# Kernel tuning notes

Hardware: AMD Instinct MI355X
Metric: run time of the kernel (lower is better)

Reference implementation:

```python
import jax, jax.numpy as jnp
import numpy as np

H = 2048          # hidden_size
NH = 16           # num_attention_heads
D_NOPE = 64
D_ROPE = 64
D_V = 64
KV_RANK = 256
E = 8             # n_routed_experts
INTER = 1408      # moe_intermediate_size
EPS = 1e-6
THETA = 10000.0
B, S = 1, 2048
Q_HEAD = D_NOPE + D_ROPE


def rms_norm(x, w, eps=EPS):
    xf = x.astype(jnp.float32)
    var = jnp.mean(xf * xf, axis=-1, keepdims=True)
    return (w * (xf * jax.lax.rsqrt(var + eps))).astype(x.dtype)


def rotate_half(x):
    d = x.shape[-1] // 2
    return jnp.concatenate([-x[..., d:], x[..., :d]], axis=-1)


def rope_tables(seq_len, dim, theta=THETA):
    inv_freq = 1.0 / (theta ** (jnp.arange(0, dim, 2, dtype=jnp.float32) / dim))
    t = jnp.arange(seq_len, dtype=jnp.float32)
    freqs = jnp.outer(t, inv_freq)
    emb = jnp.concatenate([freqs, freqs], axis=-1)  # [S, dim]
    return jnp.cos(emb), jnp.sin(emb)


def setup_inputs() -> dict:
    key = jax.random.key(0)
    ks = jax.random.split(key, 10)
    sc = 0.02
    inp = {
        "positions": jnp.broadcast_to(jnp.arange(S, dtype=jnp.int32)[None, :], (B, S)),
        "hidden_states": jax.random.normal(ks[0], (B, S, H), dtype=jnp.float32),
        "input_ln_w": jnp.ones((H,), jnp.float32),
        "q_proj_w": jax.random.normal(ks[1], (NH * Q_HEAD, H), jnp.float32) * sc,
        "kv_a_w": jax.random.normal(ks[2], (KV_RANK + D_ROPE, H), jnp.float32) * sc,
        "kv_a_ln_w": jnp.ones((KV_RANK,), jnp.float32),
        "kv_b_w": jax.random.normal(ks[3], (NH * (D_NOPE + D_V), KV_RANK), jnp.float32) * sc,
        "o_proj_w": jax.random.normal(ks[4], (H, NH * D_V), jnp.float32) * sc,
        "post_ln_w": jnp.ones((H,), jnp.float32),
        "gate_w": jax.random.normal(ks[5], (E, H), jnp.float32) * sc,
        "fc1_w": jax.random.normal(ks[6], (E, INTER, H), jnp.float32) * sc,
        "fc2_w": jax.random.normal(ks[7], (E, H, INTER), jnp.float32) * sc,
    }
    return inp


def reference(positions, hidden_states, input_ln_w, q_proj_w, kv_a_w, kv_a_ln_w,
              kv_b_w, o_proj_w, post_ln_w, gate_w, fc1_w, fc2_w):
    x = hidden_states
    sa_in = rms_norm(x, input_ln_w)

    # Q projection -> [B, NH, S, D_NOPE + D_ROPE]
    q = (sa_in @ q_proj_w.T).reshape(B, S, NH, Q_HEAD).transpose(0, 2, 1, 3)
    q_nope, q_pe = q[..., :D_NOPE], q[..., D_NOPE:]

    # KV compression path
    ckv_pe = sa_in @ kv_a_w.T                       # [B, S, KV_RANK + D_ROPE]
    compressed_kv, k_pe = ckv_pe[..., :KV_RANK], ckv_pe[..., KV_RANK:]
    k_pe = k_pe.reshape(B, S, 1, D_ROPE).transpose(0, 2, 1, 3)  # [B,1,S,Dr]
    kv = (rms_norm(compressed_kv, kv_a_ln_w) @ kv_b_w.T)
    kv = kv.reshape(B, S, NH, D_NOPE + D_V).transpose(0, 2, 1, 3)
    k_nope, v = kv[..., :D_NOPE], kv[..., D_NOPE:]

    # RoPE on pe halves
    cos, sin = rope_tables(S, D_ROPE)
    cos_sel = cos[positions][:, None]               # [B,1,S,Dr]
    sin_sel = sin[positions][:, None]
    q_pe = q_pe * cos_sel + rotate_half(q_pe) * sin_sel
    k_pe = k_pe * cos_sel + rotate_half(k_pe) * sin_sel

    query = jnp.concatenate([q_nope, q_pe], axis=-1)                       # [B,NH,S,Dq]
    key = jnp.concatenate([k_nope, jnp.broadcast_to(k_pe, (B, NH, S, D_ROPE))], axis=-1)

    scale = Q_HEAD ** -0.5
    scores = jnp.einsum("bhqd,bhkd->bhqk", query, key) * scale
    causal = jnp.tril(jnp.ones((S, S), dtype=bool))
    scores = jnp.where(causal, scores, jnp.finfo(scores.dtype).min)
    attn = jax.nn.softmax(scores, axis=-1)
    ctx = jnp.einsum("bhqk,bhkd->bhqd", attn, v)                            # [B,NH,S,Dv]
    ctx = ctx.transpose(0, 2, 1, 3).reshape(B, S, NH * D_V)
    attn_out = ctx @ o_proj_w.T

    x = x + attn_out

    # dense all-expert MoE
    mlp_in = rms_norm(x, post_ln_w)
    probs = jax.nn.softmax(mlp_in @ gate_w.T, axis=-1)                      # [B,S,E]
    h = jax.nn.silu(jnp.einsum("bsd,eid->bsei", mlp_in, fc1_w))             # [B,S,E,INTER]
    moe_out = jnp.einsum("bse,bsei,ehi->bsh", probs, h, fc2_w)

    return x + moe_out
```

## Files before the change

kernel.cpp:

```cpp
#include <hip/hip_runtime.h>
#include <cstdint>
#include <cstddef>

typedef __bf16 bf16;
typedef __bf16 bf16x8 __attribute__((ext_vector_type(8)));
typedef float  f32x4  __attribute__((ext_vector_type(4)));

constexpr int S_      = 2048;
constexpr int H_      = 2048;
constexpr int NH_     = 16;
constexpr int KV_RANK_= 256;
constexpr int EXP_    = 8;
constexpr int INTER_  = 1408;
constexpr int QH_     = 128;
constexpr float EPS_  = 1e-6f;

__device__ inline void gload16(const void* g, void* l) {
  __builtin_amdgcn_global_load_lds(
      (const __attribute__((address_space(1))) void*)g,
      (__attribute__((address_space(3))) void*)l, 16, 0, 0);
}

enum { EPI_BF16 = 0, EPI_F32 = 1, EPI_ADD = 2, EPI_SILU = 3, EPI_ATOM = 4 };

template <int EPI, typename TB, int TILE>
__global__ void __launch_bounds__(256) gemm_bt(
    const bf16* __restrict__ A, const TB* __restrict__ B,
    void* __restrict__ Cv, const float* __restrict__ aux,
    int M, int N, int K, int lda, int ldb, int ldc, int flags,
    long zA, long zB, long zC, long auxZ, int auxRS,
    int kPerE, long bExpStride, int expBasePerZ)
{
  constexpr int FR = TILE / 32;
  if ((flags & 1) && blockIdx.x > blockIdx.y) return;
  const int tileN = blockIdx.x * TILE;
  const int tileM = blockIdx.y * TILE;
  const int z = blockIdx.z;
  A += (long)z * zA;

  __shared__ __align__(16) bf16 As[TILE * 64];
  __shared__ __align__(16) TB   Bs[TILE * 64];
  char* AsB = (char*)As;
  char* BsB = (char*)Bs;

  const int tid  = threadIdx.x;
  const int lane = tid & 63;
  const int wave = tid >> 6;
  const int wr = wave >> 1, wc = wave & 1;
  const int quad = lane >> 4, r16 = lane & 15;

  const int ldbe = (kPerE > 0) ? kPerE : ldb;
  const TB* BzBase = (kPerE > 0) ? (B + (long)z * expBasePerZ * bExpStride)
                                 : (B + (long)z * zB);

  constexpr int IA = TILE / 32;
  const bf16* aG[IA]; char* aL[IA];
#pragma unroll
  for (int i = 0; i < IA; i++) {
    int n = (wave * IA + i) * 64 + lane;
    int row = n >> 3, cp = n & 7;
    int cc = (cp ^ (row & 7)) << 3;
    int rowg = tileM + row; if (rowg > M - 1) rowg = M - 1;
    aG[i] = A + (long)rowg * lda + cc;
    aL[i] = AsB + (long)(wave * IA + i) * 1024;
  }
  constexpr int IB = (sizeof(TB) == 4) ? (TILE / 16) : (TILE / 32);
  const TB* bG[IB]; char* bL[IB];
#pragma unroll
  for (int i = 0; i < IB; i++) {
    int n = (wave * IB + i) * 64 + lane;
    int row, cc;
    if constexpr (sizeof(TB) == 4) { row = n >> 4; cc = ((n & 15) ^ (row & 15)) << 2; }
    else                           { row = n >> 3; cc = ((n & 7)  ^ (row & 7))  << 3; }
    int rowg = tileN + row; if (rowg > N - 1) rowg = N - 1;
    bG[i] = BzBase + (long)rowg * ldbe + cc;
    bL[i] = BsB + (long)(wave * IB + i) * 1024;
  }

  int aOff[FR], bOff[FR];
#pragma unroll
  for (int i = 0; i < FR; i++) {
    int row = wr * (TILE / 2) + i * 16 + r16;
    aOff[i] = row * 128 + ((quad ^ (row & 7)) << 4);
  }
#pragma unroll
  for (int j = 0; j < FR; j++) {
    int row = wc * (TILE / 2) + j * 16 + r16;
    if constexpr (sizeof(TB) == 4) bOff[j] = row * 256 + (((2 * quad) ^ (row & 15)) << 4);
    else                           bOff[j] = row * 128 + ((quad ^ (row & 7)) << 4);
  }

  f32x4 acc[FR][FR];
#pragma unroll
  for (int i = 0; i < FR; i++)
#pragma unroll
    for (int j = 0; j < FR; j++)
#pragma unroll
      for (int r = 0; r < 4; r++) acc[i][j][r] = 0.f;

  const int kEnd = (flags & 2) ? (tileM + TILE < K ? tileM + TILE : K) : K;
  int bk = 0; long eOff = 0;
  for (int k0 = 0; k0 < kEnd; k0 += 64) {
#pragma unroll
    for (int i = 0; i < IA; i++) gload16(aG[i] + k0, aL[i]);
#pragma unroll
    for (int i = 0; i < IB; i++) gload16(bG[i] + eOff + bk, bL[i]);
    __syncthreads();

#pragma unroll
    for (int s = 0; s < 2; s++) {
      bf16x8 af[FR], bfv[FR];
#pragma unroll
      for (int i = 0; i < FR; i++)
        af[i] = *(const bf16x8*)(AsB + (aOff[i] ^ (s << 6)));
#pragma unroll
      for (int j = 0; j < FR; j++) {
        if constexpr (sizeof(TB) == 2) {
          bfv[j] = *(const bf16x8*)(BsB + (bOff[j] ^ (s << 6)));
        } else {
          int a0 = bOff[j] ^ (s << 7);
          f32x4 lo = *(const f32x4*)(BsB + a0);
          f32x4 hi = *(const f32x4*)(BsB + (a0 ^ 16));
          bf16x8 v;
          v[0]=(bf16)lo[0]; v[1]=(bf16)lo[1]; v[2]=(bf16)lo[2]; v[3]=(bf16)lo[3];
          v[4]=(bf16)hi[0]; v[5]=(bf16)hi[1]; v[6]=(bf16)hi[2]; v[7]=(bf16)hi[3];
          bfv[j] = v;
        }
      }
#pragma unroll
      for (int i = 0; i < FR; i++)
#pragma unroll
        for (int j = 0; j < FR; j++)
          acc[i][j] = __builtin_amdgcn_mfma_f32_16x16x32_bf16(af[i], bfv[j], acc[i][j], 0, 0, 0);
    }
    __syncthreads();

    bk += 64;
    if (kPerE > 0 && bk >= kPerE) { bk = 0; eOff += bExpStride; }
  }

  bf16*  Cb = (bf16*)Cv + (long)z * zC;
  float* Cf = (float*)Cv + (long)z * zC;
  const float* auxp = aux + (long)z * auxZ;
  const int mB = tileM + wr * (TILE / 2) + quad * 4;
  const int nB = tileN + wc * (TILE / 2) + r16;
#pragma unroll
  for (int i = 0; i < FR; i++) {
#pragma unroll
    for (int r = 0; r < 4; r++) {
      int gm = mB + i * 16 + r;
      if (gm >= M) continue;
      float rowAux = 0.f;
      if constexpr (EPI == EPI_SILU) rowAux = auxp[(long)gm * auxRS];
#pragma unroll
      for (int j = 0; j < FR; j++) {
        int gn = nB + j * 16;
        if (gn >= N) continue;
        float v = acc[i][j][r];
        long off = (long)gm * ldc + gn;
        if constexpr (EPI == EPI_BF16)      Cb[off] = (bf16)v;
        else if constexpr (EPI == EPI_F32)  Cf[off] = v;
        else if constexpr (EPI == EPI_ADD)  Cf[off] = auxp[(long)gm * auxRS + gn] + v;
        else if constexpr (EPI == EPI_SILU) { float sv = v / (1.f + __expf(-v)); Cb[off] = (bf16)(sv * rowAux); }
        else                                atomicAdd(&Cf[off], v);
      }
    }
  }
}

template <int NIT>
__global__ void __launch_bounds__(256) rmsnorm_k(
    const float* __restrict__ x, const float* __restrict__ w,
    bf16* __restrict__ out, int inStride)
{
  const int row = blockIdx.x, tid = threadIdx.x;
  const float* xr = x + (long)row * inStride;
  float vals[NIT];
  float ss = 0.f;
#pragma unroll
  for (int i = 0; i < NIT; i++) { float v = xr[i * 256 + tid]; vals[i] = v; ss += v * v; }
#pragma unroll
  for (int o = 32; o; o >>= 1) ss += __shfl_xor(ss, o, 64);
  __shared__ float red[4];
  if ((tid & 63) == 0) red[tid >> 6] = ss;
  __syncthreads();
  ss = red[0] + red[1] + red[2] + red[3];
  const float rinv = rsqrtf(ss / (float)(NIT * 256) + EPS_);
  bf16* orow = out + (long)row * (NIT * 256);
#pragma unroll
  for (int i = 0; i < NIT; i++) { int c = i * 256 + tid; orow[c] = (bf16)(w[c] * vals[i] * rinv); }
}

__global__ void prep_qkv_k(const bf16* __restrict__ q, const bf16* __restrict__ kv,
                           const float* __restrict__ ckv, const int* __restrict__ pos,
                           bf16* __restrict__ query, bf16* __restrict__ key,
                           bf16* __restrict__ vvT)
{
  const int s = blockIdx.x, h = blockIdx.y, d = threadIdx.x;
  const long qkOff = ((long)h * S_ + s) * QH_ + d;
  if (d < 64) {
    query[qkOff] = q[(long)s * H_ + h * QH_ + d];
    key[qkOff]   = kv[(long)s * H_ + h * QH_ + d];
    vvT[((long)h * 64 + d) * S_ + s] = kv[(long)s * H_ + h * QH_ + 64 + d];
  } else {
    const int i = d - 64;
    const float p = (float)pos[s];
    const float invf = powf(10000.f, -(float)(2 * (i & 31)) / 64.f);
    const float ang = p * invf;
    const float cc = cosf(ang), sn = sinf(ang);
    const float xq  = (float)q[(long)s * H_ + h * QH_ + 64 + i];
    const float xqr = (i < 32) ? -(float)q[(long)s * H_ + h * QH_ + 64 + i + 32]
                               :  (float)q[(long)s * H_ + h * QH_ + 64 + i - 32];
    query[qkOff] = (bf16)(xq * cc + xqr * sn);
    const float xk  = ckv[(long)s * 320 + 256 + i];
    const float xkr = (i < 32) ? -ckv[(long)s * 320 + 256 + i + 32]
                               :  ckv[(long)s * 320 + 256 + i - 32];
    key[qkOff] = (bf16)(xk * cc + xkr * sn);
  }
}

__global__ void __launch_bounds__(256) softmax_causal_k(bf16* __restrict__ sc, long zStride, float scale)
{
  const int row = blockIdx.x, tid = threadIdx.x;
  bf16* p = sc + (long)blockIdx.y * zStride + (long)row * S_;
  float vals[8];
  float mx = -1e30f;
#pragma unroll
  for (int i = 0; i < 8; i++) {
    int c = i * 256 + tid;
    float v = (c <= row) ? (float)p[c] * scale : -1e30f;
    vals[i] = v; mx = fmaxf(mx, v);
  }
#pragma unroll
  for (int o = 32; o; o >>= 1) mx = fmaxf(mx, __shfl_xor(mx, o, 64));
  __shared__ float redA[4], redB[4];
  if ((tid & 63) == 0) redA[tid >> 6] = mx;
  __syncthreads();
  mx = fmaxf(fmaxf(redA[0], redA[1]), fmaxf(redA[2], redA[3]));
  float sum = 0.f;
#pragma unroll
  for (int i = 0; i < 8; i++) { float e = __expf(vals[i] - mx); vals[i] = e; sum += e; }
#pragma unroll
  for (int o = 32; o; o >>= 1) sum += __shfl_xor(sum, o, 64);
  if ((tid & 63) == 0) redB[tid >> 6] = sum;
  __syncthreads();
  sum = redB[0] + redB[1] + redB[2] + redB[3];
  const float rinv = 1.f / sum;
  const int lim = ((row >> 6) + 1) << 6;
#pragma unroll
  for (int i = 0; i < 8; i++) {
    int c = i * 256 + tid;
    if (c < lim) p[c] = (bf16)((c <= row) ? vals[i] * rinv : 0.f);
  }
}

__global__ void __launch_bounds__(256) gate_k(const bf16* __restrict__ mlp,
                                              const float* __restrict__ gw,
                                              float* __restrict__ probs)
{
  const int s = blockIdx.x, tid = threadIdx.x;
  float acc[8];
#pragma unroll
  for (int e = 0; e < 8; e++) acc[e] = 0.f;
  for (int c = tid; c < H_; c += 256) {
    float x = (float)mlp[(long)s * H_ + c];
#pragma unroll
    for (int e = 0; e < 8; e++) acc[e] += x * gw[e * H_ + c];
  }
  __shared__ float red[4][8];
#pragma unroll
  for (int e = 0; e < 8; e++) {
    float v = acc[e];
#pragma unroll
    for (int o = 32; o; o >>= 1) v += __shfl_xor(v, o, 64);
    if ((tid & 63) == 0) red[tid >> 6][e] = v;
  }
  __syncthreads();
  if (tid == 0) {
    float l[8]; float mx = -1e30f;
#pragma unroll
    for (int e = 0; e < 8; e++) { l[e] = red[0][e] + red[1][e] + red[2][e] + red[3][e]; mx = fmaxf(mx, l[e]); }
    float sum = 0.f;
#pragma unroll
    for (int e = 0; e < 8; e++) { l[e] = __expf(l[e] - mx); sum += l[e]; }
    float r = 1.f / sum;
#pragma unroll
    for (int e = 0; e < 8; e++) probs[(long)s * 8 + e] = l[e] * r;
  }
}

__global__ void __launch_bounds__(256) wconv_k(const float* __restrict__ in,
                                               bf16* __restrict__ out, int n8)
{
  int i = blockIdx.x * 256 + threadIdx.x;
  if (i < n8) {
    f32x4 a = ((const f32x4*)in)[2 * i];
    f32x4 b = ((const f32x4*)in)[2 * i + 1];
    bf16x8 v;
    v[0] = (bf16)a[0]; v[1] = (bf16)a[1]; v[2] = (bf16)a[2]; v[3] = (bf16)a[3];
    v[4] = (bf16)b[0]; v[5] = (bf16)b[1]; v[6] = (bf16)b[2]; v[7] = (bf16)b[3];
    ((bf16x8*)out)[i] = v;
  }
}

extern "C" void kernel_launch(void* const* d_in, const int* in_sizes, int n_in,
                              void* d_out, int out_size, void* d_ws, size_t ws_size,
                              hipStream_t stream)
{
  const int*   positions = (const int*)  d_in[0];
  const float* hidden    = (const float*)d_in[1];
  const float* ln1       = (const float*)d_in[2];
  const float* wq        = (const float*)d_in[3];
  const float* wkva      = (const float*)d_in[4];
  const float* lnkv      = (const float*)d_in[5];
  const float* wkvb      = (const float*)d_in[6];
  const float* wo        = (const float*)d_in[7];
  const float* ln2       = (const float*)d_in[8];
  const float* wg        = (const float*)d_in[9];
  const float* wfc1      = (const float*)d_in[10];
  const float* wfc2      = (const float*)d_in[11];
  float* out = (float*)d_out;

  char* wsb = (char*)d_ws;
  size_t off = 0;
  auto alloc = [&](size_t bytes) -> void* {
    void* p = wsb + off;
    off += (bytes + 255) & ~(size_t)255;
    return p;
  };
  bf16*  sa_in = (bf16*) alloc((size_t)S_ * H_ * 2);
  bf16*  qb    = (bf16*) alloc((size_t)S_ * H_ * 2);
  float* ckv   = (float*)alloc((size_t)S_ * 320 * 4);
  bf16*  ckvn  = (bf16*) alloc((size_t)S_ * KV_RANK_ * 2);
  bf16*  kvb   = (bf16*) alloc((size_t)S_ * H_ * 2);
  bf16*  query = (bf16*) alloc((size_t)NH_ * S_ * QH_ * 2);
  bf16*  key   = (bf16*) alloc((size_t)NH_ * S_ * QH_ * 2);
  bf16*  vvT   = (bf16*) alloc((size_t)NH_ * 64 * S_ * 2);
  bf16*  ctx   = (bf16*) alloc((size_t)S_ * NH_ * 64 * 2);
  bf16*  mlp   = (bf16*) alloc((size_t)S_ * H_ * 2);
  float* probs = (float*)alloc((size_t)S_ * 8 * 4);
  bf16*  hbuf  = (bf16*) alloc((size_t)S_ * EXP_ * INTER_ * 2);

  const size_t MBy = (size_t)1 << 20;
  const size_t rem = (ws_size > off) ? ws_size - off : 0;
  const size_t szSS   = (size_t)S_ * S_ * 2;
  const size_t szMoeW = (size_t)EXP_ * INTER_ * H_ * 2;

  int tier;
  if      (rem >= 136 * MBy) tier = 1;
  else if (rem >=  94 * MBy) tier = 2;
  else                       tier = 3;
  const bool cw = (tier <= 2);
  const int nz = (tier == 1) ? 16 : (tier == 2 ? 4 : 1);

  char* R = (char*)alloc(tier == 1 ? 16 * szSS : (tier == 2 ? 2 * szMoeW : szSS));
  bf16* scores = (bf16*)R;
  bf16* fc1b   = (bf16*)R;
  bf16* fc2b   = (bf16*)(R + szMoeW);
  bf16* wqb   = (bf16*)hbuf;
  bf16* wkvab = wqb   + (size_t)H_ * H_;
  bf16* wkvbb = wkvab + (size_t)320 * H_;
  bf16* wob   = wkvbb + (size_t)H_ * KV_RANK_;

  const float scale = 0.08838834764831845f;
  const long zQ = (long)S_ * QH_, zS = (long)S_ * S_, zV = (long)64 * S_;

  rmsnorm_k<8><<<S_, 256, 0, stream>>>(hidden, ln1, sa_in, H_);

  if (cw) {
    wconv_k<<<(H_*H_/8 + 255)/256, 256, 0, stream>>>(wq, wqb, H_*H_/8);
    wconv_k<<<(320*H_/8 + 255)/256, 256, 0, stream>>>(wkva, wkvab, 320*H_/8);
    wconv_k<<<(H_*KV_RANK_/8 + 255)/256, 256, 0, stream>>>(wkvb, wkvbb, H_*KV_RANK_/8);
    wconv_k<<<(H_*NH_*64/8 + 255)/256, 256, 0, stream>>>(wo, wob, H_*NH_*64/8);
  }

  if (cw) gemm_bt<EPI_BF16, bf16, 64><<<dim3(32,32,1), 256, 0, stream>>>(
      sa_in, wqb, qb, hidden, S_, H_, H_, H_, H_, H_, 0, 0,0,0,0,0, 0,0,0);
  else    gemm_bt<EPI_BF16, float, 64><<<dim3(32,32,1), 256, 0, stream>>>(
      sa_in, wq,  qb, hidden, S_, H_, H_, H_, H_, H_, 0, 0,0,0,0,0, 0,0,0);

  if (cw) gemm_bt<EPI_F32, bf16, 64><<<dim3(5,32,1), 256, 0, stream>>>(
      sa_in, wkvab, ckv, hidden, S_, 320, H_, H_, H_, 320, 0, 0,0,0,0,0, 0,0,0);
  else    gemm_bt<EPI_F32, float, 64><<<dim3(5,32,1), 256, 0, stream>>>(
      sa_in, wkva,  ckv, hidden, S_, 320, H_, H_, H_, 320, 0, 0,0,0,0,0, 0,0,0);

  rmsnorm_k<1><<<S_, 256, 0, stream>>>(ckv, lnkv, ckvn, 320);

  if (cw) gemm_bt<EPI_BF16, bf16, 64><<<dim3(32,32,1), 256, 0, stream>>>(
      ckvn, wkvbb, kvb, hidden, S_, H_, KV_RANK_, KV_RANK_, KV_RANK_, H_, 0, 0,0,0,0,0, 0,0,0);
  else    gemm_bt<EPI_BF16, float, 64><<<dim3(32,32,1), 256, 0, stream>>>(
      ckvn, wkvb,  kvb, hidden, S_, H_, KV_RANK_, KV_RANK_, KV_RANK_, H_, 0, 0,0,0,0,0, 0,0,0);

  prep_qkv_k<<<dim3(S_, NH_), 128, 0, stream>>>(qb, kvb, ckv, positions, query, key, vvT);

  for (int l = 0; l < NH_ / nz; l++) {
    gemm_bt<EPI_BF16, bf16, 128><<<dim3(16,16,nz), 256, 0, stream>>>(
        query + (long)l*nz*zQ, key + (long)l*nz*zQ, scores, hidden,
        S_, S_, QH_, QH_, QH_, S_, 1, zQ, zQ, zS, 0,0, 0,0,0);
    softmax_causal_k<<<dim3(S_, nz), 256, 0, stream>>>(scores, zS, scale);
    gemm_bt<EPI_BF16, bf16, 64><<<dim3(1,32,nz), 256, 0, stream>>>(
        scores, vvT + (long)l*nz*zV, ctx + (long)l*nz*64, hidden,
        S_, 64, S_, S_, S_, NH_*64, 2, zS, zV, 64, 0,0, 0,0,0);
  }

  if (cw) {
    wconv_k<<<(EXP_*INTER_*H_/8 + 255)/256, 256, 0, stream>>>(wfc1, fc1b, EXP_*INTER_*H_/8);
    wconv_k<<<(EXP_*INTER_*H_/8 + 255)/256, 256, 0, stream>>>(wfc2, fc2b, EXP_*INTER_*H_/8);
  }

  if (cw) gemm_bt<EPI_ADD, bf16, 64><<<dim3(32,32,1), 256, 0, stream>>>(
      ctx, wob, out, hidden, S_, H_, NH_*64, NH_*64, NH_*64, H_, 0, 0,0,0,0, H_, 0,0,0);
  else    gemm_bt<EPI_ADD, float, 64><<<dim3(32,32,1), 256, 0, stream>>>(
      ctx, wo,  out, hidden, S_, H_, NH_*64, NH_*64, NH_*64, H_, 0, 0,0,0,0, H_, 0,0,0);

  rmsnorm_k<8><<<S_, 256, 0, stream>>>(out, ln2, mlp, H_);
  gate_k<<<S_, 256, 0, stream>>>(mlp, wg, probs);

  if (cw) gemm_bt<EPI_SILU, bf16, 128><<<dim3(11,16,8), 256, 0, stream>>>(
      mlp, fc1b, hbuf, probs, S_, INTER_, H_, H_, H_, EXP_*INTER_, 0,
      0, (long)INTER_*H_, INTER_, 1, 8, 0, 0, 0);
  else    gemm_bt<EPI_SILU, float, 128><<<dim3(11,16,8), 256, 0, stream>>>(
      mlp, wfc1, hbuf, probs, S_, INTER_, H_, H_, H_, EXP_*INTER_, 0,
      0, (long)INTER_*H_, INTER_, 1, 8, 0, 0, 0);

  if (cw) gemm_bt<EPI_ATOM, bf16, 128><<<dim3(16,16,4), 256, 0, stream>>>(
      hbuf, fc2b, out, hidden, S_, H_, 2*INTER_, EXP_*INTER_, 0, H_, 0,
      (long)2*INTER_, 0, 0, 0, 0, INTER_, (long)H_*INTER_, 2);
  else    gemm_bt<EPI_ATOM, float, 128><<<dim3(16,16,4), 256, 0, stream>>>(
      hbuf, wfc2, out, hidden, S_, H_, 2*INTER_, EXP_*INTER_, 0, H_, 0,
      (long)2*INTER_, 0, 0, 0, 0, INTER_, (long)H_*INTER_, 2);
}
```

Before: 790.6 us.

## Replace materialized attention with fused flash-attention kernel and restructure workspace

Replaces the per-head scores GEMM, causal softmax kernel and probs@V GEMM with one fused flash-attention kernel that keeps scores in registers and LDS, using online softmax over 64-key tiles with causal early exit. This removes the S×S score buffer traffic and the extra launches, which in turn frees workspace so the bf16 MoE weight copies can always be allocated. The fc2 GEMM split changes from 4 z-slices of 2 experts each to 8 single-expert slices accumulated atomically, and gemm_bt gets a launch-bounds occupancy hint. The flash kernel launches one block per 64-row query tile per head, so per-block work is unbalanced; the grid order reverses query tiles so the longest ones start first.

```diff
diff --git a/kernel.cpp b/kernel.cpp
--- a/kernel.cpp
+++ b/kernel.cpp
@@ -24,15 +24,14 @@
 enum { EPI_BF16 = 0, EPI_F32 = 1, EPI_ADD = 2, EPI_SILU = 3, EPI_ATOM = 4 };
 
 template <int EPI, typename TB, int TILE>
-__global__ void __launch_bounds__(256) gemm_bt(
+__global__ void __launch_bounds__(256, 3) gemm_bt(
     const bf16* __restrict__ A, const TB* __restrict__ B,
     void* __restrict__ Cv, const float* __restrict__ aux,
-    int M, int N, int K, int lda, int ldb, int ldc, int flags,
+    int M, int N, int K, int lda, int ldb, int ldc,
     long zA, long zB, long zC, long auxZ, int auxRS,
     int kPerE, long bExpStride, int expBasePerZ)
 {
   constexpr int FR = TILE / 32;
-  if ((flags & 1) && blockIdx.x > blockIdx.y) return;
   const int tileN = blockIdx.x * TILE;
   const int tileM = blockIdx.y * TILE;
   const int z = blockIdx.z;
@@ -98,9 +97,8 @@
 #pragma unroll
       for (int r = 0; r < 4; r++) acc[i][j][r] = 0.f;
 
-  const int kEnd = (flags & 2) ? (tileM + TILE < K ? tileM + TILE : K) : K;
   int bk = 0; long eOff = 0;
-  for (int k0 = 0; k0 < kEnd; k0 += 64) {
+  for (int k0 = 0; k0 < K; k0 += 64) {
 #pragma unroll
     for (int i = 0; i < IA; i++) gload16(aG[i] + k0, aL[i]);
 #pragma unroll
@@ -165,6 +163,140 @@
         else                                atomicAdd(&Cf[off], v);
       }
     }
+  }
+}
+
+__global__ void __launch_bounds__(256) flash_k(
+    const bf16* __restrict__ q, const bf16* __restrict__ k,
+    const bf16* __restrict__ vt, bf16* __restrict__ ctx, float scale)
+{
+  const int h  = blockIdx.x;
+  const int qt = (int)gridDim.y - 1 - (int)blockIdx.y;
+  const int tid = threadIdx.x, lane = tid & 63, wave = tid >> 6;
+  const int quad = lane >> 4, r16 = lane & 15;
+
+  __shared__ __align__(16) bf16 Ks[64 * 128];
+  __shared__ __align__(16) bf16 Vs[64 * 64];
+  __shared__ __align__(16) bf16 Ps[4][16 * 64];
+  char* KsB = (char*)Ks;
+  char* VsB = (char*)Vs;
+  char* PsB = (char*)&Ps[wave][0];
+
+  bf16x8 qf[4];
+  {
+    const bf16* qp = q + ((long)h * S_ + qt * 64 + wave * 16 + r16) * 128 + quad * 8;
+#pragma unroll
+    for (int ks = 0; ks < 4; ks++) qf[ks] = *(const bf16x8*)(qp + ks * 32);
+  }
+
+  const bf16* kG[4]; char* kL[4];
+#pragma unroll
+  for (int i = 0; i < 4; i++) {
+    int n = (wave * 4 + i) * 64 + lane;
+    int row = n >> 4, c = n & 15;
+    kG[i] = k + ((long)h * S_ + row) * 128 + ((c ^ (row & 15)) << 3);
+    kL[i] = KsB + (long)(wave * 4 + i) * 1024;
+  }
+  const bf16* vG[2]; char* vL[2];
+#pragma unroll
+  for (int i = 0; i < 2; i++) {
+    int n = (wave * 2 + i) * 64 + lane;
+    int row = n >> 3, c = n & 7;
+    vG[i] = vt + ((long)h * 64 + row) * S_ + ((c ^ (row & 7)) << 3);
+    vL[i] = VsB + (long)(wave * 2 + i) * 1024;
+  }
+
+  float mr[4], lr[4];
+#pragma unroll
+  for (int r = 0; r < 4; r++) { mr[r] = -1e30f; lr[r] = 0.f; }
+  f32x4 o[4];
+#pragma unroll
+  for (int j = 0; j < 4; j++)
+#pragma unroll
+    for (int r = 0; r < 4; r++) o[j][r] = 0.f;
+
+  for (int kt = 0; kt <= qt; kt++) {
+#pragma unroll
+    for (int i = 0; i < 4; i++) gload16(kG[i] + (long)kt * 64 * 128, kL[i]);
+#pragma unroll
+    for (int i = 0; i < 2; i++) gload16(vG[i] + kt * 64, vL[i]);
+    __syncthreads();
+
+    f32x4 s[4];
+#pragma unroll
+    for (int j = 0; j < 4; j++)
+#pragma unroll
+      for (int r = 0; r < 4; r++) s[j][r] = 0.f;
+#pragma unroll
+    for (int ks = 0; ks < 4; ks++) {
+#pragma unroll
+      for (int j = 0; j < 4; j++) {
+        int row = j * 16 + r16;
+        int c = ks * 4 + quad;
+        bf16x8 bfr = *(const bf16x8*)(KsB + row * 256 + ((c ^ (row & 15)) << 4));
+        s[j] = __builtin_amdgcn_mfma_f32_16x16x32_bf16(qf[ks], bfr, s[j], 0, 0, 0);
+      }
+    }
+
+    if (kt == qt) {
+#pragma unroll
+      for (int j = 0; j < 4; j++)
+#pragma unroll
+        for (int r = 0; r < 4; r++)
+          if (j * 16 + r16 > wave * 16 + quad * 4 + r) s[j][r] = -1e30f;
+    }
+
+    float pj[4][4];
+#pragma unroll
+    for (int r = 0; r < 4; r++) {
+      float mx = fmaxf(fmaxf(s[0][r], s[1][r]), fmaxf(s[2][r], s[3][r]));
+#pragma unroll
+      for (int off = 1; off < 16; off <<= 1) mx = fmaxf(mx, __shfl_xor(mx, off, 64));
+      mx *= scale;
+      float nm = fmaxf(mr[r], mx);
+      float alpha = __expf(mr[r] - nm);
+      mr[r] = nm;
+      float rs = 0.f;
+#pragma unroll
+      for (int j = 0; j < 4; j++) { float e = __expf(s[j][r] * scale - nm); pj[j][r] = e; rs += e; }
+#pragma unroll
+      for (int off = 1; off < 16; off <<= 1) rs += __shfl_xor(rs, off, 64);
+      lr[r] = lr[r] * alpha + rs;
+#pragma unroll
+      for (int j = 0; j < 4; j++) o[j][r] *= alpha;
+    }
+
+#pragma unroll
+    for (int j = 0; j < 4; j++) {
+      int chunk = j * 2 + (r16 >> 3);
+#pragma unroll
+      for (int r = 0; r < 4; r++) {
+        int row = quad * 4 + r;
+        *(bf16*)(PsB + row * 128 + ((chunk ^ (row & 7)) << 4) + ((r16 & 7) << 1)) = (bf16)pj[j][r];
+      }
+    }
+
+#pragma unroll
+    for (int ks = 0; ks < 2; ks++) {
+      int c = ks * 4 + quad;
+      bf16x8 af = *(const bf16x8*)(PsB + r16 * 128 + ((c ^ (r16 & 7)) << 4));
+#pragma unroll
+      for (int j = 0; j < 4; j++) {
+        int row = j * 16 + r16;
+        bf16x8 bfr = *(const bf16x8*)(VsB + row * 128 + ((c ^ (row & 7)) << 4));
+        o[j] = __builtin_amdgcn_mfma_f32_16x16x32_bf16(af, bfr, o[j], 0, 0, 0);
+      }
+    }
+    __syncthreads();
+  }
+
+  bf16* cp = ctx + ((long)(qt * 64 + wave * 16 + quad * 4)) * (NH_ * 64) + h * 64 + r16;
+#pragma unroll
+  for (int r = 0; r < 4; r++) {
+    float rl = 1.f / lr[r];
+#pragma unroll
+    for (int j = 0; j < 4; j++)
+      cp[(long)r * NH_ * 64 + j * 16] = (bf16)(o[j][r] * rl);
   }
 }
 
@@ -219,41 +351,6 @@
   }
 }
 
-__global__ void __launch_bounds__(256) softmax_causal_k(bf16* __restrict__ sc, long zStride, float scale)
-{
-  const int row = blockIdx.x, tid = threadIdx.x;
-  bf16* p = sc + (long)blockIdx.y * zStride + (long)row * S_;
-  float vals[8];
-  float mx = -1e30f;
-#pragma unroll
-  for (int i = 0; i < 8; i++) {
-    int c = i * 256 + tid;
-    float v = (c <= row) ? (float)p[c] * scale : -1e30f;
-    vals[i] = v; mx = fmaxf(mx, v);
-  }
-#pragma unroll
-  for (int o = 32; o; o >>= 1) mx = fmaxf(mx, __shfl_xor(mx, o, 64));
-  __shared__ float redA[4], redB[4];
-  if ((tid & 63) == 0) redA[tid >> 6] = mx;
-  __syncthreads();
-  mx = fmaxf(fmaxf(redA[0], redA[1]), fmaxf(redA[2], redA[3]));
-  float sum = 0.f;
-#pragma unroll
-  for (int i = 0; i < 8; i++) { float e = __expf(vals[i] - mx); vals[i] = e; sum += e; }
-#pragma unroll
-  for (int o = 32; o; o >>= 1) sum += __shfl_xor(sum, o, 64);
-  if ((tid & 63) == 0) redB[tid >> 6] = sum;
-  __syncthreads();
-  sum = redB[0] + redB[1] + redB[2] + redB[3];
-  const float rinv = 1.f / sum;
-  const int lim = ((row >> 6) + 1) << 6;
-#pragma unroll
-  for (int i = 0; i < 8; i++) {
-    int c = i * 256 + tid;
-    if (c < lim) p[c] = (bf16)((c <= row) ? vals[i] * rinv : 0.f);
-  }
-}
-
 __global__ void __launch_bounds__(256) gate_k(const bf16* __restrict__ mlp,
                                               const float* __restrict__ gw,
                                               float* __restrict__ probs)
@@ -343,27 +440,17 @@
 
   const size_t MBy = (size_t)1 << 20;
   const size_t rem = (ws_size > off) ? ws_size - off : 0;
-  const size_t szSS   = (size_t)S_ * S_ * 2;
   const size_t szMoeW = (size_t)EXP_ * INTER_ * H_ * 2;
-
-  int tier;
-  if      (rem >= 136 * MBy) tier = 1;
-  else if (rem >=  94 * MBy) tier = 2;
-  else                       tier = 3;
-  const bool cw = (tier <= 2);
-  const int nz = (tier == 1) ? 16 : (tier == 2 ? 4 : 1);
-
-  char* R = (char*)alloc(tier == 1 ? 16 * szSS : (tier == 2 ? 2 * szMoeW : szSS));
-  bf16* scores = (bf16*)R;
-  bf16* fc1b   = (bf16*)R;
-  bf16* fc2b   = (bf16*)(R + szMoeW);
+  const bool cw = (rem >= 93 * MBy);
+
+  bf16* fc1b = nullptr; bf16* fc2b = nullptr;
+  if (cw) { fc1b = (bf16*)alloc(szMoeW); fc2b = (bf16*)alloc(szMoeW); }
   bf16* wqb   = (bf16*)hbuf;
   bf16* wkvab = wqb   + (size_t)H_ * H_;
   bf16* wkvbb = wkvab + (size_t)320 * H_;
   bf16* wob   = wkvbb + (size_t)H_ * KV_RANK_;
 
   const float scale = 0.08838834764831845f;
-  const long zQ = (long)S_ * QH_, zS = (long)S_ * S_, zV = (long)64 * S_;
 
   rmsnorm_k<8><<<S_, 256, 0, stream>>>(hidden, ln1, sa_in, H_);
 
@@ -372,61 +459,50 @@
     wconv_k<<<(320*H_/8 + 255)/256, 256, 0, stream>>>(wkva, wkvab, 320*H_/8);
     wconv_k<<<(H_*KV_RANK_/8 + 255)/256, 256, 0, stream>>>(wkvb, wkvbb, H_*KV_RANK_/8);
     wconv_k<<<(H_*NH_*64/8 + 255)/256, 256, 0, stream>>>(wo, wob, H_*NH_*64/8);
-  }
-
-  if (cw) gemm_bt<EPI_BF16, bf16, 64><<<dim3(32,32,1), 256, 0, stream>>>(
-      sa_in, wqb, qb, hidden, S_, H_, H_, H_, H_, H_, 0, 0,0,0,0,0, 0,0,0);
-  else    gemm_bt<EPI_BF16, float, 64><<<dim3(32,32,1), 256, 0, stream>>>(
-      sa_in, wq,  qb, hidden, S_, H_, H_, H_, H_, H_, 0, 0,0,0,0,0, 0,0,0);
-
-  if (cw) gemm_bt<EPI_F32, bf16, 64><<<dim3(5,32,1), 256, 0, stream>>>(
-      sa_in, wkvab, ckv, hidden, S_, 320, H_, H_, H_, 320, 0, 0,0,0,0,0, 0,0,0);
-  else    gemm_bt<EPI_F32, float, 64><<<dim3(5,32,1), 256, 0, stream>>>(
-      sa_in, wkva,  ckv, hidden, S_, 320, H_, H_, H_, 320, 0, 0,0,0,0,0, 0,0,0);
-
-  rmsnorm_k<1><<<S_, 256, 0, stream>>>(ckv, lnkv, ckvn, 320);
-
-  if (cw) gemm_bt<EPI_BF16, bf16, 64><<<dim3(32,32,1), 256, 0, stream>>>(
-      ckvn, wkvbb, kvb, hidden, S_, H_, KV_RANK_, KV_RANK_, KV_RANK_, H_, 0, 0,0,0,0,0, 0,0,0);
-  else    gemm_bt<EPI_BF16, float, 64><<<dim3(32,32,1), 256, 0, stream>>>(
-      ckvn, wkvb,  kvb, hidden, S_, H_, KV_RANK_, KV_RANK_, KV_RANK_, H_, 0, 0,0,0,0,0, 0,0,0);
-
-  prep_qkv_k<<<dim3(S_, NH_), 128, 0, stream>>>(qb, kvb, ckv, positions, query, key, vvT);
-
-  for (int l = 0; l < NH_ / nz; l++) {
-    gemm_bt<EPI_BF16, bf16, 128><<<dim3(16,16,nz), 256, 0, stream>>>(
-        query + (long)l*nz*zQ, key + (long)l*nz*zQ, scores, hidden,
-        S_, S_, QH_, QH_, QH_, S_, 1, zQ, zQ, zS, 0,0, 0,0,0);
-    softmax_causal_k<<<dim3(S_, nz), 256, 0, stream>>>(scores, zS, scale);
-    gemm_bt<EPI_BF16, bf16, 64><<<dim3(1,32,nz), 256, 0, stream>>>(
-        scores, vvT + (long)l*nz*zV, ctx + (long)l*nz*64, hidden,
-        S_, 64, S_, S_, S_, NH_*64, 2, zS, zV, 64, 0,0, 0,0,0);
-  }
-
-  if (cw) {
     wconv_k<<<(EXP_*INTER_*H_/8 + 255)/256, 256, 0, stream>>>(wfc1, fc1b, EXP_*INTER_*H_/8);
     wconv_k<<<(EXP_*INTER_*H_/8 + 255)/256, 256, 0, stream>>>(wfc2, fc2b, EXP_*INTER_*H_/8);
   }
 
+  if (cw) gemm_bt<EPI_BF16, bf16, 64><<<dim3(32,32,1), 256, 0, stream>>>(
+      sa_in, wqb, qb, hidden, S_, H_, H_, H_, H_, H_, 0,0,0,0,0, 0,0,0);
+  else    gemm_bt<EPI_BF16, float, 64><<<dim3(32,32,1), 256, 0, stream>>>(
+      sa_in, wq,  qb, hidden, S_, H_, H_, H_, H_, H_, 0,0,0,0,0, 0,0,0);
+
+  if (cw) gemm_bt<EPI_F32, bf16, 64><<<dim3(5,32,1), 256, 0, stream>>>(
+      sa_in, wkvab, ckv, hidden, S_, 320, H_, H_, H_, 320, 0,0,0,0,0, 0,0,0);
+  else    gemm_bt<EPI_F32, float, 64><<<dim3(5,32,1), 256, 0, stream>>>(
+      sa_in, wkva,  ckv, hidden, S_, 320, H_, H_, H_, 320, 0,0,0,0,0, 0,0,0);
+
+  rmsnorm_k<1><<<S_, 256, 0, stream>>>(ckv, lnkv, ckvn, 320);
+
+  if (cw) gemm_bt<EPI_BF16, bf16, 64><<<dim3(32,32,1), 256, 0, stream>>>(
+      ckvn, wkvbb, kvb, hidden, S_, H_, KV_RANK_, KV_RANK_, KV_RANK_, H_, 0,0,0,0,0, 0,0,0);
+  else    gemm_bt<EPI_BF16, float, 64><<<dim3(32,32,1), 256, 0, stream>>>(
+      ckvn, wkvb,  kvb, hidden, S_, H_, KV_RANK_, KV_RANK_, KV_RANK_, H_, 0,0,0,0,0, 0,0,0);
+
+  prep_qkv_k<<<dim3(S_, NH_), 128, 0, stream>>>(qb, kvb, ckv, positions, query, key, vvT);
+
+  flash_k<<<dim3(NH_, S_/64), 256, 0, stream>>>(query, key, vvT, ctx, scale);
+
   if (cw) gemm_bt<EPI_ADD, bf16, 64><<<dim3(32,32,1), 256, 0, stream>>>(
-      ctx, wob, out, hidden, S_, H_, NH_*64, NH_*64, NH_*64, H_, 0, 0,0,0,0, H_, 0,0,0);
+      ctx, wob, out, hidden, S_, H_, NH_*64, NH_*64, NH_*64, H_, 0,0,0,0, H_, 0,0,0);
   else    gemm_bt<EPI_ADD, float, 64><<<dim3(32,32,1), 256, 0, stream>>>(
-      ctx, wo,  out, hidden, S_, H_, NH_*64, NH_*64, NH_*64, H_, 0, 0,0,0,0, H_, 0,0,0);
+      ctx, wo,  out, hidden, S_, H_, NH_*64, NH_*64, NH_*64, H_, 0,0,0,0, H_, 0,0,0);
 
   rmsnorm_k<8><<<S_, 256, 0, stream>>>(out, ln2, mlp, H_);
   gate_k<<<S_, 256, 0, stream>>>(mlp, wg, probs);
 
   if (cw) gemm_bt<EPI_SILU, bf16, 128><<<dim3(11,16,8), 256, 0, stream>>>(
-      mlp, fc1b, hbuf, probs, S_, INTER_, H_, H_, H_, EXP_*INTER_, 0,
+      mlp, fc1b, hbuf, probs, S_, INTER_, H_, H_, H_, EXP_*INTER_,
       0, (long)INTER_*H_, INTER_, 1, 8, 0, 0, 0);
   else    gemm_bt<EPI_SILU, float, 128><<<dim3(11,16,8), 256, 0, stream>>>(
-      mlp, wfc1, hbuf, probs, S_, INTER_, H_, H_, H_, EXP_*INTER_, 0,
+      mlp, wfc1, hbuf, probs, S_, INTER_, H_, H_, H_, EXP_*INTER_,
       0, (long)INTER_*H_, INTER_, 1, 8, 0, 0, 0);
 
-  if (cw) gemm_bt<EPI_ATOM, bf16, 128><<<dim3(16,16,4), 256, 0, stream>>>(
-      hbuf, fc2b, out, hidden, S_, H_, 2*INTER_, EXP_*INTER_, 0, H_, 0,
-      (long)2*INTER_, 0, 0, 0, 0, INTER_, (long)H_*INTER_, 2);
-  else    gemm_bt<EPI_ATOM, float, 128><<<dim3(16,16,4), 256, 0, stream>>>(
-      hbuf, wfc2, out, hidden, S_, H_, 2*INTER_, EXP_*INTER_, 0, H_, 0,
-      (long)2*INTER_, 0, 0, 0, 0, INTER_, (long)H_*INTER_, 2);
-}
+  if (cw) gemm_bt<EPI_ATOM, bf16, 128><<<dim3(16,16,8), 256, 0, stream>>>(
+      hbuf, fc2b, out, hidden, S_, H_, INTER_, EXP_*INTER_, 0, H_,
+      (long)INTER_, 0, 0, 0, 0, INTER_, (long)H_*INTER_, 1);
+  else    gemm_bt<EPI_ATOM, float, 128><<<dim3(16,16,8), 256, 0, stream>>>(
+      hbuf, wfc2, out, hidden, S_, H_, INTER_, EXP_*INTER_, 0, H_,
+      (long)INTER_, 0, 0, 0, 0, INTER_, (long)H_*INTER_, 1);
+}
```

Result: faster. 748.1 us (-5.4%).
